# Performance work log

Measured on AMD Instinct MI355X. Metric: run time of the kernel, lower is better.

## Reference

```python
import jax, jax.numpy as jnp
import numpy as np

B = 256          # number of graphs
D = 256          # hidden_dim
H = 4            # num_heads
S = 4            # num_seeds
DH = D // H      # head dim = 64
MAX_NODES = 2048 # max nodes per graph (padding target)


def setup_inputs() -> dict:
    key = jax.random.key(0)
    ks = jax.random.split(key, 8)
    # per-graph node counts, constructed so they sum exactly to B*1024 = 262144
    rng = np.random.RandomState(0)
    delta = rng.randint(0, 960, size=B // 2)
    counts = np.concatenate([1024 + delta, 1024 - delta]).astype(np.int32)
    N = int(counts.sum())  # 262144
    return {
        "node_feat": jax.random.normal(ks[0], (N, D), dtype=jnp.float32),
        "batch_num_nodes": jnp.asarray(counts),
        "seeds": jax.random.normal(ks[1], (S, D), dtype=jnp.float32),
        "in_proj_w": jax.random.normal(ks[2], (3 * D, D), dtype=jnp.float32) * 0.02,
        "in_proj_b": jnp.zeros((3 * D,), jnp.float32),
        "out_proj_w": jax.random.normal(ks[3], (D, D), dtype=jnp.float32) * 0.02,
        "out_proj_b": jnp.zeros((D,), jnp.float32),
        "fc1_w": jax.random.normal(ks[4], (D, S * D), dtype=jnp.float32) * 0.02,
        "fc1_b": jnp.zeros((D,), jnp.float32),
        "fc2_w": jax.random.normal(ks[5], (D, D), dtype=jnp.float32) * 0.02,
        "fc2_b": jnp.zeros((D,), jnp.float32),
    }


def reference(node_feat, batch_num_nodes, seeds, in_proj_w, in_proj_b,
              out_proj_w, out_proj_b, fc1_w, fc1_b, fc2_w, fc2_b):
    N = node_feat.shape[0]
    counts = batch_num_nodes
    # ragged -> padded [B, MAX_NODES, D] via scatter (equiv. of split + zero-pad + stack)
    offsets = jnp.concatenate([jnp.zeros((1,), counts.dtype), jnp.cumsum(counts)[:-1]])
    gid = jnp.repeat(jnp.arange(B, dtype=counts.dtype), counts, total_repeat_length=N)
    pos = jnp.arange(N, dtype=counts.dtype) - offsets[gid]
    padded = jnp.zeros((B, MAX_NODES, D), node_feat.dtype).at[gid, pos].set(node_feat)
    pad_mask = jnp.arange(MAX_NODES)[None, :] >= counts[:, None]  # True = padding key

    # torch nn.MultiheadAttention: packed in_proj split into q/k/v
    Wq, Wk, Wv = jnp.split(in_proj_w, 3, axis=0)
    bq, bk, bv = jnp.split(in_proj_b, 3)
    q = (seeds @ Wq.T + bq).reshape(S, H, DH)                 # [S,H,DH] (broadcast over B)
    k = (padded @ Wk.T + bk).reshape(B, MAX_NODES, H, DH)     # [B,M,H,DH]
    v = (padded @ Wv.T + bv).reshape(B, MAX_NODES, H, DH)

    scale = 1.0 / jnp.sqrt(jnp.asarray(DH, q.dtype))
    scores = jnp.einsum('shd,bmhd->bhsm', q, k) * scale       # [B,H,S,M]
    scores = jnp.where(pad_mask[:, None, None, :], jnp.asarray(-1e9, scores.dtype), scores)
    attn = jax.nn.softmax(scores, axis=-1)
    ctx = jnp.einsum('bhsm,bmhd->bshd', attn, v).reshape(B, S, D)
    attended = ctx @ out_proj_w.T + out_proj_b                # [B,S,D]

    # output_proj: Linear(S*D, D) -> GELU(exact) -> Linear(D, D)
    flat = attended.reshape(B, S * D)
    h = jax.nn.gelu(flat @ fc1_w.T + fc1_b, approximate=False)
    return h @ fc2_w.T + fc2_b                                # [B,D]
```

## Files before the change

### kernel.cpp

```cpp
#include <hip/hip_runtime.h>

#define D 256
#define SH 16
#define Ss 4
#define CH 256
#define NT 64
#define XS_STRIDE 272
#define WB_STRIDE 80

typedef _Float16 half8 __attribute__((ext_vector_type(8)));
typedef _Float16 half4 __attribute__((ext_vector_type(4)));
typedef float f32x4 __attribute__((ext_vector_type(4)));

#define OFF_AF16   ((size_t)0)
#define OFF_CM     ((size_t)8192)
#define OFF_Q      ((size_t)8448)
#define OFF_DESC   ((size_t)12544)
#define OFF_SUMEXP ((size_t)33280)
#define OFF_ACC    ((size_t)49664)
#define OFF_WVT    ((size_t)4243968)
#define OFF_WOT    ((size_t)4506112)
#define OFF_FC1T   ((size_t)4768256)
#define OFF_FC2T   ((size_t)5816832)

__global__ void k_prep(const float* __restrict__ seeds,
                       const float* __restrict__ inw,
                       const float* __restrict__ inb,
                       const int* __restrict__ counts,
                       char* __restrict__ ws) {
  int t = threadIdx.x;
  if (blockIdx.x < 4) {
    int s = blockIdx.x;
    __shared__ float sv[D];
    sv[t] = seeds[s * D + t];
    __syncthreads();
    const float4* wr = (const float4*)(inw + (size_t)t * D);
    float acc = inb[t];
    #pragma unroll 8
    for (int j = 0; j < 64; j++) {
      float4 w4 = wr[j];
      acc += w4.x * sv[4*j] + w4.y * sv[4*j+1] + w4.z * sv[4*j+2] + w4.w * sv[4*j+3];
    }
    ((float*)(ws + OFF_Q))[s * D + t] = acc;
  } else {
    __shared__ int s1[256], s2[256];
    int cnt = counts[t];
    int nch = (cnt + CH - 1) / CH;
    s1[t] = cnt; s2[t] = nch;
    __syncthreads();
    for (int off = 1; off < 256; off <<= 1) {
      int a1 = (t >= off) ? s1[t - off] : 0;
      int a2 = (t >= off) ? s2[t - off] : 0;
      __syncthreads();
      s1[t] += a1; s2[t] += a2;
      __syncthreads();
    }
    int start = s1[t] - cnt, cb = s2[t] - nch;
    int4* desc = (int4*)(ws + OFF_DESC + 16);
    for (int j = 0; j < nch; j++) {
      int nn = cnt - j * CH; if (nn > CH) nn = CH;
      desc[cb + j] = make_int4(t, start + j * CH, nn, 0);
    }
    if (t == 255) *(int*)(ws + OFF_DESC) = s2[255];
  }
}

__global__ void k_mk_a(const float* __restrict__ inw, char* __restrict__ ws) {
  int sh = blockIdx.x;
  int s = sh >> 2, h = sh & 3;
  int j = threadIdx.x;
  __shared__ float qh[64];
  __shared__ float red[256];
  if (j < 64) qh[j] = ((const float*)(ws + OFF_Q))[s * D + h * 64 + j];
  __syncthreads();
  const float* wk = inw + (size_t)(D + h * 64) * D;
  float a = 0.f;
  #pragma unroll 8
  for (int d = 0; d < 64; d++) a += qh[d] * wk[(size_t)d * D + j];
  a *= 0.125f;
  ((_Float16*)(ws + OFF_AF16))[sh * D + j] = (_Float16)a;
  red[j] = a * a;
  __syncthreads();
  for (int st = 128; st > 0; st >>= 1) { if (j < st) red[j] += red[j + st]; __syncthreads(); }
  if (j == 0) ((float*)(ws + OFF_CM))[sh] = -6.0f * sqrtf(red[0]);
}

__global__ void k_transpose(const float* __restrict__ inw, const float* __restrict__ ow,
                            const float* __restrict__ f1w, const float* __restrict__ f2w,
                            char* __restrict__ ws) {
  int b = blockIdx.x;
  const float* src; float* dst; int R, C, ti, tj;
  if (b < 64)       { src = inw + (size_t)512 * D; dst = (float*)(ws + OFF_WVT);  R = 256; C = 256;  int x = b;        tj = x / 8;  ti = x % 8; }
  else if (b < 128) { src = ow;                    dst = (float*)(ws + OFF_WOT);  R = 256; C = 256;  int x = b - 64;   tj = x / 8;  ti = x % 8; }
  else if (b < 192) { src = f2w;                   dst = (float*)(ws + OFF_FC2T); R = 256; C = 256;  int x = b - 128;  tj = x / 8;  ti = x % 8; }
  else              { src = f1w;                   dst = (float*)(ws + OFF_FC1T); R = 256; C = 1024; int x = b - 192;  tj = x / 8;  ti = x % 8; }
  __shared__ float tl[32][33];
  int tx = threadIdx.x & 31, ty = threadIdx.x >> 5;
  #pragma unroll
  for (int k = 0; k < 4; k++) {
    int r = ty + k * 8;
    tl[r][tx] = src[(size_t)(ti * 32 + r) * C + tj * 32 + tx];
  }
  __syncthreads();
  #pragma unroll
  for (int k = 0; k < 4; k++) {
    int r = ty + k * 8;
    dst[(size_t)(tj * 32 + r) * R + ti * 32 + tx] = tl[tx][r];
  }
}

__launch_bounds__(256, 4)
__global__ void k_main(const float* __restrict__ nf, char* __restrict__ ws) {
  int nchunks = *(const int*)(ws + OFF_DESC);
  if ((int)blockIdx.x >= nchunks) return;
  int4 dsc = ((const int4*)(ws + OFF_DESC + 16))[blockIdx.x];
  int g = dsc.x, start = dsc.y, cnt = dsc.z;

  __shared__ _Float16 xs[NT * XS_STRIDE];
  __shared__ _Float16 wb[SH * WB_STRIDE];

  int t = threadIdx.x;
  int lane = t & 63, wv = t >> 6;
  int col = lane & 15, q = lane >> 4;

  const _Float16* af = (const _Float16*)(ws + OFF_AF16);
  half8 aw[8];
  #pragma unroll
  for (int kc = 0; kc < 8; kc++) aw[kc] = *(const half8*)(af + col * D + kc * 32 + q * 8);
  float cmv = ((const float*)(ws + OFF_CM))[col];

  f32x4 acc[4] = {{0,0,0,0},{0,0,0,0},{0,0,0,0},{0,0,0,0}};
  float dsum = 0.f;

  int ntile = (cnt + NT - 1) / NT;
  for (int tile = 0; tile < ntile; tile++) {
    #pragma unroll 4
    for (int p = 0; p < 16; p++) {
      int flat = p * 256 + t;
      int row = flat >> 6, c4 = flat & 63;
      int nloc = tile * NT + row;
      float4 v = make_float4(0.f, 0.f, 0.f, 0.f);
      if (nloc < cnt) v = ((const float4*)(nf + (size_t)(start + nloc) * D))[c4];
      half4 hv;
      hv[0] = (_Float16)v.x; hv[1] = (_Float16)v.y; hv[2] = (_Float16)v.z; hv[3] = (_Float16)v.w;
      *(half4*)(xs + row * XS_STRIDE + c4 * 4) = hv;
    }
    __syncthreads();

    f32x4 sc = {0, 0, 0, 0};
    const _Float16* xrow = xs + (wv * 16 + col) * XS_STRIDE + q * 8;
    #pragma unroll
    for (int kc = 0; kc < 8; kc++) {
      half8 xa = *(const half8*)(xrow + kc * 32);
      sc = __builtin_amdgcn_mfma_f32_16x16x32_f16(xa, aw[kc], sc, 0, 0, 0);
    }
    #pragma unroll
    for (int r = 0; r < 4; r++) {
      int nloc = wv * 16 + q * 4 + r;
      float arg = fminf(sc[r] + cmv, 10.f);
      float wj = (tile * NT + nloc < cnt) ? __expf(arg) : 0.f;
      _Float16 wh = (_Float16)wj;
      dsum += (float)wh;
      wb[col * WB_STRIDE + nloc] = wh;
    }
    __syncthreads();

    #pragma unroll
    for (int ks = 0; ks < 2; ks++) {
      half8 wa = *(const half8*)(wb + col * WB_STRIDE + ks * 32 + q * 8);
      #pragma unroll
      for (int dt = 0; dt < 4; dt++) {
        int dd = wv * 64 + dt * 16 + col;
        half8 xb;
        #pragma unroll
        for (int jj = 0; jj < 8; jj++) xb[jj] = xs[(ks * 32 + q * 8 + jj) * XS_STRIDE + dd];
        acc[dt] = __builtin_amdgcn_mfma_f32_16x16x32_f16(wa, xb, acc[dt], 0, 0, 0);
      }
    }
    __syncthreads();
  }

  dsum += __shfl_xor(dsum, 16);
  dsum += __shfl_xor(dsum, 32);
  if (q == 0) atomicAdd(((float*)(ws + OFF_SUMEXP)) + g * SH + col, dsum);
  float* accw = (float*)(ws + OFF_ACC);
  #pragma unroll
  for (int dt = 0; dt < 4; dt++)
    #pragma unroll
    for (int r = 0; r < 4; r++)
      atomicAdd(&accw[(size_t)(g * SH + q * 4 + r) * D + wv * 64 + dt * 16 + col], acc[dt][r]);
}

__global__ void k_final(const float* __restrict__ inb, const float* __restrict__ ob,
                        const float* __restrict__ f1b, const float* __restrict__ f2b,
                        const char* __restrict__ ws, float* __restrict__ out) {
  int t = threadIdx.x;
  int g0 = blockIdx.x * 2;
  const float* sume = (const float*)(ws + OFF_SUMEXP);
  const float* accw = (const float*)(ws + OFF_ACC);
  const float* WvT = (const float*)(ws + OFF_WVT);
  const float* WoT = (const float*)(ws + OFF_WOT);
  const float* F1T = (const float*)(ws + OFF_FC1T);
  const float* F2T = (const float*)(ws + OFF_FC2T);

  __shared__ float xb2[2][SH][D];
  __shared__ float cx2[2][Ss][D];
  __shared__ float fl2[2][1024];
  __shared__ float hh2[2][D];
  __shared__ float inv[32];

  if (t < 32) inv[t] = 1.0f / sume[(g0 + (t >> 4)) * SH + (t & 15)];
  __syncthreads();
  for (int e = t; e < 2 * SH * D; e += 256) {
    int gg = e >> 12, sh = (e >> 8) & 15, d = e & 255;
    xb2[gg][sh][d] = accw[(size_t)(g0 + gg) * SH * D + sh * D + d] * inv[gg * 16 + sh];
  }
  __syncthreads();

  {
    float ca[2][4] = {{0,0,0,0},{0,0,0,0}};
    int h = t >> 6;
    for (int d = 0; d < D; d++) {
      float wvd = WvT[(size_t)d * D + t];
      #pragma unroll
      for (int gg = 0; gg < 2; gg++)
        #pragma unroll
        for (int s = 0; s < 4; s++)
          ca[gg][s] += wvd * xb2[gg][s * 4 + h][d];
    }
    float bv = inb[2 * D + t];
    #pragma unroll
    for (int gg = 0; gg < 2; gg++)
      #pragma unroll
      for (int s = 0; s < 4; s++) cx2[gg][s][t] = ca[gg][s] + bv;
  }
  __syncthreads();
  {
    float aa[2][4] = {{0,0,0,0},{0,0,0,0}};
    for (int d = 0; d < D; d++) {
      float wod = WoT[(size_t)d * D + t];
      #pragma unroll
      for (int gg = 0; gg < 2; gg++)
        #pragma unroll
        for (int s = 0; s < 4; s++)
          aa[gg][s] += wod * cx2[gg][s][d];
    }
    float bo = ob[t];
    #pragma unroll
    for (int gg = 0; gg < 2; gg++)
      #pragma unroll
      for (int s = 0; s < 4; s++) fl2[gg][s * D + t] = aa[gg][s] + bo;
  }
  __syncthreads();
  {
    float f1[2] = {0, 0};
    for (int k = 0; k < 1024; k++) {
      float w1 = F1T[(size_t)k * D + t];
      f1[0] += w1 * fl2[0][k];
      f1[1] += w1 * fl2[1][k];
    }
    #pragma unroll
    for (int gg = 0; gg < 2; gg++) {
      float x = f1[gg] + f1b[t];
      hh2[gg][t] = 0.5f * x * (1.0f + erff(x * 0.70710678118654752f));
    }
  }
  __syncthreads();
  {
    float f2[2] = {0, 0};
    for (int d = 0; d < D; d++) {
      float w2 = F2T[(size_t)d * D + t];
      f2[0] += w2 * hh2[0][d];
      f2[1] += w2 * hh2[1][d];
    }
    #pragma unroll
    for (int gg = 0; gg < 2; gg++) out[(size_t)(g0 + gg) * D + t] = f2[gg] + f2b[t];
  }
}

extern "C" void kernel_launch(void* const* d_in, const int* in_sizes, int n_in,
                              void* d_out, int out_size, void* d_ws, size_t ws_size,
                              hipStream_t stream) {
  const float* nf    = (const float*)d_in[0];
  const int*   cnts  = (const int*)d_in[1];
  const float* seeds = (const float*)d_in[2];
  const float* inw   = (const float*)d_in[3];
  const float* inb   = (const float*)d_in[4];
  const float* ow    = (const float*)d_in[5];
  const float* obv   = (const float*)d_in[6];
  const float* f1w   = (const float*)d_in[7];
  const float* f1b   = (const float*)d_in[8];
  const float* f2w   = (const float*)d_in[9];
  const float* f2b   = (const float*)d_in[10];
  char* ws = (char*)d_ws;
  float* out = (float*)d_out;
  int N = in_sizes[0] / D;

  hipMemsetAsync(ws + OFF_SUMEXP, 0, (size_t)16384 + 4194304, stream);
  k_prep<<<5, 256, 0, stream>>>(seeds, inw, inb, cnts, ws);
  k_mk_a<<<16, 256, 0, stream>>>(inw, ws);
  k_transpose<<<448, 256, 0, stream>>>(inw, ow, f1w, f2w, ws);
  int maxc = (N + CH - 1) / CH + 256;
  k_main<<<maxc, 256, 0, stream>>>(nf, ws);
  k_final<<<128, 256, 0, stream>>>(inb, obv, f1b, f2b, ws, out);
}
```

Measured before the change: 550.1 us.

## Fuse all stages into one persistent cooperative kernel with grid syncs

Replaces the memset and five separate launches with a single cooperative kernel. It zeroes the workspace, runs prep, query-key precompute and weight transposes, then processes chunks in a grid-stride loop and does the final MLP one graph per block, with grid.sync between phases. The aim is to remove launch gaps and the tail imbalance of the chunk kernel. In exchange the grid is fixed at the occupancy-bounded block count (assumes 256 CUs), and the final stage uses only 256 blocks with one graph each, so the transposed weights are read twice as often.

```diff
diff --git a/kernel.cpp b/kernel.cpp
--- a/kernel.cpp
+++ b/kernel.cpp
@@ -1,4 +1,7 @@
 #include <hip/hip_runtime.h>
+#include <hip/hip_cooperative_groups.h>
+
+namespace cg = cooperative_groups;
 
 #define D 256
 #define SH 16
@@ -14,7 +17,6 @@
 
 #define OFF_AF16   ((size_t)0)
 #define OFF_CM     ((size_t)8192)
-#define OFF_Q      ((size_t)8448)
 #define OFF_DESC   ((size_t)12544)
 #define OFF_SUMEXP ((size_t)33280)
 #define OFF_ACC    ((size_t)49664)
@@ -23,27 +25,88 @@
 #define OFF_FC1T   ((size_t)4768256)
 #define OFF_FC2T   ((size_t)5816832)
 
-__global__ void k_prep(const float* __restrict__ seeds,
-                       const float* __restrict__ inw,
-                       const float* __restrict__ inb,
-                       const int* __restrict__ counts,
-                       char* __restrict__ ws) {
-  int t = threadIdx.x;
-  if (blockIdx.x < 4) {
-    int s = blockIdx.x;
-    __shared__ float sv[D];
-    sv[t] = seeds[s * D + t];
-    __syncthreads();
-    const float4* wr = (const float4*)(inw + (size_t)t * D);
-    float acc = inb[t];
+#define SMEM_BYTES (NT * XS_STRIDE * 2 + SH * WB_STRIDE * 2)
+
+__launch_bounds__(256, 4)
+__global__ void k_all(const float* __restrict__ nf,
+                      const int* __restrict__ counts,
+                      const float* __restrict__ seeds,
+                      const float* __restrict__ inw,
+                      const float* __restrict__ inb,
+                      const float* __restrict__ ow,
+                      const float* __restrict__ obv,
+                      const float* __restrict__ f1w,
+                      const float* __restrict__ f1b,
+                      const float* __restrict__ f2w,
+                      const float* __restrict__ f2b,
+                      char* __restrict__ ws,
+                      float* __restrict__ out) {
+  __shared__ __align__(16) char smem[SMEM_BYTES];
+  cg::grid_group grid = cg::this_grid();
+  const int t = threadIdx.x;
+  const int b = blockIdx.x;
+  const int nblk = gridDim.x;
+
+  {
+    f32x4* z = (f32x4*)(ws + OFF_SUMEXP);
+    const int total4 = (16384 + 4194304) / 16;
+    f32x4 zero = {0.f, 0.f, 0.f, 0.f};
+    for (int i = b * 256 + t; i < total4; i += nblk * 256) z[i] = zero;
+  }
+
+  if (b < 448) {
+    const float* src; float* dst; int R, C, ti, tj;
+    if (b < 64)       { src = inw + (size_t)512 * D; dst = (float*)(ws + OFF_WVT);  R = 256; C = 256;  int x = b;       tj = x / 8; ti = x % 8; }
+    else if (b < 128) { src = ow;                    dst = (float*)(ws + OFF_WOT);  R = 256; C = 256;  int x = b - 64;  tj = x / 8; ti = x % 8; }
+    else if (b < 192) { src = f2w;                   dst = (float*)(ws + OFF_FC2T); R = 256; C = 256;  int x = b - 128; tj = x / 8; ti = x % 8; }
+    else              { src = f1w;                   dst = (float*)(ws + OFF_FC1T); R = 256; C = 1024; int x = b - 192; tj = x / 8; ti = x % 8; }
+    float (*tl)[33] = (float(*)[33])smem;
+    int tx = t & 31, ty = t >> 5;
+    #pragma unroll
+    for (int k = 0; k < 4; k++) {
+      int r = ty + k * 8;
+      tl[r][tx] = src[(size_t)(ti * 32 + r) * C + tj * 32 + tx];
+    }
+    __syncthreads();
+    #pragma unroll
+    for (int k = 0; k < 4; k++) {
+      int r = ty + k * 8;
+      dst[(size_t)(tj * 32 + r) * R + ti * 32 + tx] = tl[tx][r];
+    }
+  } else if (b < 464) {
+    int sh = b - 448, s = sh >> 2, h = sh & 3;
+    float* sd   = (float*)smem;
+    float* part = sd + 256;
+    float* qh   = part + 256;
+    float* red  = qh + 64;
+    sd[t] = seeds[s * D + t];
+    __syncthreads();
+    int j = t & 63, p = t >> 6;
+    const float4* wq = (const float4*)(inw + (size_t)(h * 64 + j) * D + p * 64);
+    float pa = 0.f;
+    #pragma unroll
+    for (int k4 = 0; k4 < 16; k4++) {
+      float4 w4 = wq[k4];
+      pa += w4.x * sd[p*64 + 4*k4] + w4.y * sd[p*64 + 4*k4 + 1]
+          + w4.z * sd[p*64 + 4*k4 + 2] + w4.w * sd[p*64 + 4*k4 + 3];
+    }
+    part[p * 64 + j] = pa;
+    __syncthreads();
+    if (t < 64) qh[t] = part[t] + part[64 + t] + part[128 + t] + part[192 + t] + inb[h * 64 + t];
+    __syncthreads();
+    const float* wk = inw + (size_t)(D + h * 64) * D;
+    float a = 0.f;
     #pragma unroll 8
-    for (int j = 0; j < 64; j++) {
-      float4 w4 = wr[j];
-      acc += w4.x * sv[4*j] + w4.y * sv[4*j+1] + w4.z * sv[4*j+2] + w4.w * sv[4*j+3];
-    }
-    ((float*)(ws + OFF_Q))[s * D + t] = acc;
-  } else {
-    __shared__ int s1[256], s2[256];
+    for (int d = 0; d < 64; d++) a += qh[d] * wk[(size_t)d * D + t];
+    a *= 0.125f;
+    ((_Float16*)(ws + OFF_AF16))[sh * D + t] = (_Float16)a;
+    red[t] = a * a;
+    __syncthreads();
+    for (int st = 128; st > 0; st >>= 1) { if (t < st) red[t] += red[t + st]; __syncthreads(); }
+    if (t == 0) ((float*)(ws + OFF_CM))[sh] = -6.0f * sqrtf(red[0]);
+  } else if (b == 464) {
+    int* s1 = (int*)smem;
+    int* s2 = s1 + 256;
     int cnt = counts[t];
     int nch = (cnt + CH - 1) / CH;
     s1[t] = cnt; s2[t] = nch;
@@ -57,224 +120,173 @@
     }
     int start = s1[t] - cnt, cb = s2[t] - nch;
     int4* desc = (int4*)(ws + OFF_DESC + 16);
-    for (int j = 0; j < nch; j++) {
-      int nn = cnt - j * CH; if (nn > CH) nn = CH;
-      desc[cb + j] = make_int4(t, start + j * CH, nn, 0);
+    for (int jj = 0; jj < nch; jj++) {
+      int nn = cnt - jj * CH; if (nn > CH) nn = CH;
+      desc[cb + jj] = make_int4(t, start + jj * CH, nn, 0);
     }
     if (t == 255) *(int*)(ws + OFF_DESC) = s2[255];
   }
-}
-
-__global__ void k_mk_a(const float* __restrict__ inw, char* __restrict__ ws) {
-  int sh = blockIdx.x;
-  int s = sh >> 2, h = sh & 3;
-  int j = threadIdx.x;
-  __shared__ float qh[64];
-  __shared__ float red[256];
-  if (j < 64) qh[j] = ((const float*)(ws + OFF_Q))[s * D + h * 64 + j];
-  __syncthreads();
-  const float* wk = inw + (size_t)(D + h * 64) * D;
-  float a = 0.f;
-  #pragma unroll 8
-  for (int d = 0; d < 64; d++) a += qh[d] * wk[(size_t)d * D + j];
-  a *= 0.125f;
-  ((_Float16*)(ws + OFF_AF16))[sh * D + j] = (_Float16)a;
-  red[j] = a * a;
-  __syncthreads();
-  for (int st = 128; st > 0; st >>= 1) { if (j < st) red[j] += red[j + st]; __syncthreads(); }
-  if (j == 0) ((float*)(ws + OFF_CM))[sh] = -6.0f * sqrtf(red[0]);
-}
-
-__global__ void k_transpose(const float* __restrict__ inw, const float* __restrict__ ow,
-                            const float* __restrict__ f1w, const float* __restrict__ f2w,
-                            char* __restrict__ ws) {
-  int b = blockIdx.x;
-  const float* src; float* dst; int R, C, ti, tj;
-  if (b < 64)       { src = inw + (size_t)512 * D; dst = (float*)(ws + OFF_WVT);  R = 256; C = 256;  int x = b;        tj = x / 8;  ti = x % 8; }
-  else if (b < 128) { src = ow;                    dst = (float*)(ws + OFF_WOT);  R = 256; C = 256;  int x = b - 64;   tj = x / 8;  ti = x % 8; }
-  else if (b < 192) { src = f2w;                   dst = (float*)(ws + OFF_FC2T); R = 256; C = 256;  int x = b - 128;  tj = x / 8;  ti = x % 8; }
-  else              { src = f1w;                   dst = (float*)(ws + OFF_FC1T); R = 256; C = 1024; int x = b - 192;  tj = x / 8;  ti = x % 8; }
-  __shared__ float tl[32][33];
-  int tx = threadIdx.x & 31, ty = threadIdx.x >> 5;
-  #pragma unroll
-  for (int k = 0; k < 4; k++) {
-    int r = ty + k * 8;
-    tl[r][tx] = src[(size_t)(ti * 32 + r) * C + tj * 32 + tx];
-  }
-  __syncthreads();
-  #pragma unroll
-  for (int k = 0; k < 4; k++) {
-    int r = ty + k * 8;
-    dst[(size_t)(tj * 32 + r) * R + ti * 32 + tx] = tl[tx][r];
-  }
-}
-
-__launch_bounds__(256, 4)
-__global__ void k_main(const float* __restrict__ nf, char* __restrict__ ws) {
-  int nchunks = *(const int*)(ws + OFF_DESC);
-  if ((int)blockIdx.x >= nchunks) return;
-  int4 dsc = ((const int4*)(ws + OFF_DESC + 16))[blockIdx.x];
-  int g = dsc.x, start = dsc.y, cnt = dsc.z;
-
-  __shared__ _Float16 xs[NT * XS_STRIDE];
-  __shared__ _Float16 wb[SH * WB_STRIDE];
-
-  int t = threadIdx.x;
-  int lane = t & 63, wv = t >> 6;
-  int col = lane & 15, q = lane >> 4;
-
-  const _Float16* af = (const _Float16*)(ws + OFF_AF16);
-  half8 aw[8];
-  #pragma unroll
-  for (int kc = 0; kc < 8; kc++) aw[kc] = *(const half8*)(af + col * D + kc * 32 + q * 8);
-  float cmv = ((const float*)(ws + OFF_CM))[col];
-
-  f32x4 acc[4] = {{0,0,0,0},{0,0,0,0},{0,0,0,0},{0,0,0,0}};
-  float dsum = 0.f;
-
-  int ntile = (cnt + NT - 1) / NT;
-  for (int tile = 0; tile < ntile; tile++) {
-    #pragma unroll 4
-    for (int p = 0; p < 16; p++) {
-      int flat = p * 256 + t;
-      int row = flat >> 6, c4 = flat & 63;
-      int nloc = tile * NT + row;
-      float4 v = make_float4(0.f, 0.f, 0.f, 0.f);
-      if (nloc < cnt) v = ((const float4*)(nf + (size_t)(start + nloc) * D))[c4];
-      half4 hv;
-      hv[0] = (_Float16)v.x; hv[1] = (_Float16)v.y; hv[2] = (_Float16)v.z; hv[3] = (_Float16)v.w;
-      *(half4*)(xs + row * XS_STRIDE + c4 * 4) = hv;
-    }
-    __syncthreads();
-
-    f32x4 sc = {0, 0, 0, 0};
-    const _Float16* xrow = xs + (wv * 16 + col) * XS_STRIDE + q * 8;
-    #pragma unroll
-    for (int kc = 0; kc < 8; kc++) {
-      half8 xa = *(const half8*)(xrow + kc * 32);
-      sc = __builtin_amdgcn_mfma_f32_16x16x32_f16(xa, aw[kc], sc, 0, 0, 0);
-    }
-    #pragma unroll
-    for (int r = 0; r < 4; r++) {
-      int nloc = wv * 16 + q * 4 + r;
-      float arg = fminf(sc[r] + cmv, 10.f);
-      float wj = (tile * NT + nloc < cnt) ? __expf(arg) : 0.f;
-      _Float16 wh = (_Float16)wj;
-      dsum += (float)wh;
-      wb[col * WB_STRIDE + nloc] = wh;
-    }
-    __syncthreads();
-
-    #pragma unroll
-    for (int ks = 0; ks < 2; ks++) {
-      half8 wa = *(const half8*)(wb + col * WB_STRIDE + ks * 32 + q * 8);
+
+  __threadfence();
+  grid.sync();
+  __threadfence();
+
+  {
+    _Float16* xs = (_Float16*)smem;
+    _Float16* wb = (_Float16*)(smem + NT * XS_STRIDE * 2);
+    const int lane = t & 63, wv = t >> 6;
+    const int col = lane & 15, q = lane >> 4;
+
+    const _Float16* af = (const _Float16*)(ws + OFF_AF16);
+    half8 aw[8];
+    #pragma unroll
+    for (int kc = 0; kc < 8; kc++) aw[kc] = *(const half8*)(af + col * D + kc * 32 + q * 8);
+    const float cmv = ((const float*)(ws + OFF_CM))[col];
+    const int nchunks = *(const int*)(ws + OFF_DESC);
+    float* sume = (float*)(ws + OFF_SUMEXP);
+    float* accw = (float*)(ws + OFF_ACC);
+    const int4* descp = (const int4*)(ws + OFF_DESC + 16);
+
+    for (int c = b; c < nchunks; c += nblk) {
+      int4 dsc = descp[c];
+      int g = dsc.x, start = dsc.y, cnt = dsc.z;
+
+      f32x4 acc[4] = {{0,0,0,0},{0,0,0,0},{0,0,0,0},{0,0,0,0}};
+      float dsum = 0.f;
+
+      int ntile = (cnt + NT - 1) / NT;
+      for (int tile = 0; tile < ntile; tile++) {
+        #pragma unroll 4
+        for (int p = 0; p < 16; p++) {
+          int flat = p * 256 + t;
+          int row = flat >> 6, c4 = flat & 63;
+          int nloc = tile * NT + row;
+          float4 v = make_float4(0.f, 0.f, 0.f, 0.f);
+          if (nloc < cnt) v = ((const float4*)(nf + (size_t)(start + nloc) * D))[c4];
+          half4 hv;
+          hv[0] = (_Float16)v.x; hv[1] = (_Float16)v.y; hv[2] = (_Float16)v.z; hv[3] = (_Float16)v.w;
+          *(half4*)(xs + row * XS_STRIDE + c4 * 4) = hv;
+        }
+        __syncthreads();
+
+        f32x4 sc = {0, 0, 0, 0};
+        const _Float16* xrow = xs + (wv * 16 + col) * XS_STRIDE + q * 8;
+        #pragma unroll
+        for (int kc = 0; kc < 8; kc++) {
+          half8 xa = *(const half8*)(xrow + kc * 32);
+          sc = __builtin_amdgcn_mfma_f32_16x16x32_f16(xa, aw[kc], sc, 0, 0, 0);
+        }
+        #pragma unroll
+        for (int r = 0; r < 4; r++) {
+          int nloc = wv * 16 + q * 4 + r;
+          float arg = fminf(sc[r] + cmv, 10.f);
+          float wj = (tile * NT + nloc < cnt) ? __expf(arg) : 0.f;
+          _Float16 wh = (_Float16)wj;
+          dsum += (float)wh;
+          wb[col * WB_STRIDE + nloc] = wh;
+        }
+        __syncthreads();
+
+        #pragma unroll
+        for (int ks = 0; ks < 2; ks++) {
+          half8 wa = *(const half8*)(wb + col * WB_STRIDE + ks * 32 + q * 8);
+          #pragma unroll
+          for (int dt = 0; dt < 4; dt++) {
+            int dd = wv * 64 + dt * 16 + col;
+            half8 xb;
+            #pragma unroll
+            for (int jj = 0; jj < 8; jj++) xb[jj] = xs[(ks * 32 + q * 8 + jj) * XS_STRIDE + dd];
+            acc[dt] = __builtin_amdgcn_mfma_f32_16x16x32_f16(wa, xb, acc[dt], 0, 0, 0);
+          }
+        }
+        __syncthreads();
+      }
+
+      float ds = dsum;
+      ds += __shfl_xor(ds, 16);
+      ds += __shfl_xor(ds, 32);
+      if (q == 0) atomicAdd(sume + g * SH + col, ds);
       #pragma unroll
-      for (int dt = 0; dt < 4; dt++) {
-        int dd = wv * 64 + dt * 16 + col;
-        half8 xb;
-        #pragma unroll
-        for (int jj = 0; jj < 8; jj++) xb[jj] = xs[(ks * 32 + q * 8 + jj) * XS_STRIDE + dd];
-        acc[dt] = __builtin_amdgcn_mfma_f32_16x16x32_f16(wa, xb, acc[dt], 0, 0, 0);
-      }
-    }
-    __syncthreads();
-  }
-
-  dsum += __shfl_xor(dsum, 16);
-  dsum += __shfl_xor(dsum, 32);
-  if (q == 0) atomicAdd(((float*)(ws + OFF_SUMEXP)) + g * SH + col, dsum);
-  float* accw = (float*)(ws + OFF_ACC);
-  #pragma unroll
-  for (int dt = 0; dt < 4; dt++)
-    #pragma unroll
-    for (int r = 0; r < 4; r++)
-      atomicAdd(&accw[(size_t)(g * SH + q * 4 + r) * D + wv * 64 + dt * 16 + col], acc[dt][r]);
-}
-
-__global__ void k_final(const float* __restrict__ inb, const float* __restrict__ ob,
-                        const float* __restrict__ f1b, const float* __restrict__ f2b,
-                        const char* __restrict__ ws, float* __restrict__ out) {
-  int t = threadIdx.x;
-  int g0 = blockIdx.x * 2;
-  const float* sume = (const float*)(ws + OFF_SUMEXP);
-  const float* accw = (const float*)(ws + OFF_ACC);
-  const float* WvT = (const float*)(ws + OFF_WVT);
-  const float* WoT = (const float*)(ws + OFF_WOT);
-  const float* F1T = (const float*)(ws + OFF_FC1T);
-  const float* F2T = (const float*)(ws + OFF_FC2T);
-
-  __shared__ float xb2[2][SH][D];
-  __shared__ float cx2[2][Ss][D];
-  __shared__ float fl2[2][1024];
-  __shared__ float hh2[2][D];
-  __shared__ float inv[32];
-
-  if (t < 32) inv[t] = 1.0f / sume[(g0 + (t >> 4)) * SH + (t & 15)];
-  __syncthreads();
-  for (int e = t; e < 2 * SH * D; e += 256) {
-    int gg = e >> 12, sh = (e >> 8) & 15, d = e & 255;
-    xb2[gg][sh][d] = accw[(size_t)(g0 + gg) * SH * D + sh * D + d] * inv[gg * 16 + sh];
-  }
-  __syncthreads();
-
-  {
-    float ca[2][4] = {{0,0,0,0},{0,0,0,0}};
-    int h = t >> 6;
-    for (int d = 0; d < D; d++) {
-      float wvd = WvT[(size_t)d * D + t];
+      for (int dt = 0; dt < 4; dt++)
+        #pragma unroll
+        for (int r = 0; r < 4; r++)
+          atomicAdd(&accw[(size_t)(g * SH + q * 4 + r) * D + wv * 64 + dt * 16 + col], acc[dt][r]);
+    }
+  }
+
+  __threadfence();
+  grid.sync();
+  __threadfence();
+
+  if (b < 256) {
+    const int g = b;
+    const float* sume = (const float*)(ws + OFF_SUMEXP);
+    const float* accw = (const float*)(ws + OFF_ACC);
+    const float* WvT = (const float*)(ws + OFF_WVT);
+    const float* WoT = (const float*)(ws + OFF_WOT);
+    const float* F1T = (const float*)(ws + OFF_FC1T);
+    const float* F2T = (const float*)(ws + OFF_FC2T);
+    float* xb  = (float*)smem;
+    float* cx  = xb + 16 * 256;
+    float* fl  = cx + 4 * 256;
+    float* hh  = fl + 1024;
+    float* inv = hh + 256;
+
+    if (t < 16) inv[t] = 1.0f / sume[g * SH + t];
+    __syncthreads();
+    #pragma unroll
+    for (int sh = 0; sh < 16; sh++)
+      xb[sh * 256 + t] = accw[(size_t)g * (SH * D) + sh * D + t] * inv[sh];
+    __syncthreads();
+
+    const int h = t >> 6;
+    {
+      float ca[4] = {0, 0, 0, 0};
+      #pragma unroll 4
+      for (int d = 0; d < 256; d++) {
+        float wvd = WvT[(size_t)d * D + t];
+        #pragma unroll
+        for (int s = 0; s < 4; s++) ca[s] += wvd * xb[(s * 4 + h) * 256 + d];
+      }
+      float bv = inb[2 * D + t];
       #pragma unroll
-      for (int gg = 0; gg < 2; gg++)
-        #pragma unroll
-        for (int s = 0; s < 4; s++)
-          ca[gg][s] += wvd * xb2[gg][s * 4 + h][d];
-    }
-    float bv = inb[2 * D + t];
-    #pragma unroll
-    for (int gg = 0; gg < 2; gg++)
+      for (int s = 0; s < 4; s++) cx[s * 256 + t] = ca[s] + bv;
+    }
+    __syncthreads();
+    {
+      float aa[4] = {0, 0, 0, 0};
+      #pragma unroll 4
+      for (int d = 0; d < 256; d++) {
+        float wod = WoT[(size_t)d * D + t];
+        #pragma unroll
+        for (int s = 0; s < 4; s++) aa[s] += wod * cx[s * 256 + d];
+      }
+      float bo = obv[t];
       #pragma unroll
-      for (int s = 0; s < 4; s++) cx2[gg][s][t] = ca[gg][s] + bv;
-  }
-  __syncthreads();
-  {
-    float aa[2][4] = {{0,0,0,0},{0,0,0,0}};
-    for (int d = 0; d < D; d++) {
-      float wod = WoT[(size_t)d * D + t];
-      #pragma unroll
-      for (int gg = 0; gg < 2; gg++)
-        #pragma unroll
-        for (int s = 0; s < 4; s++)
-          aa[gg][s] += wod * cx2[gg][s][d];
-    }
-    float bo = ob[t];
-    #pragma unroll
-    for (int gg = 0; gg < 2; gg++)
-      #pragma unroll
-      for (int s = 0; s < 4; s++) fl2[gg][s * D + t] = aa[gg][s] + bo;
-  }
-  __syncthreads();
-  {
-    float f1[2] = {0, 0};
-    for (int k = 0; k < 1024; k++) {
-      float w1 = F1T[(size_t)k * D + t];
-      f1[0] += w1 * fl2[0][k];
-      f1[1] += w1 * fl2[1][k];
-    }
-    #pragma unroll
-    for (int gg = 0; gg < 2; gg++) {
-      float x = f1[gg] + f1b[t];
-      hh2[gg][t] = 0.5f * x * (1.0f + erff(x * 0.70710678118654752f));
-    }
-  }
-  __syncthreads();
-  {
-    float f2[2] = {0, 0};
-    for (int d = 0; d < D; d++) {
-      float w2 = F2T[(size_t)d * D + t];
-      f2[0] += w2 * hh2[0][d];
-      f2[1] += w2 * hh2[1][d];
-    }
-    #pragma unroll
-    for (int gg = 0; gg < 2; gg++) out[(size_t)(g0 + gg) * D + t] = f2[gg] + f2b[t];
+      for (int s = 0; s < 4; s++) fl[s * 256 + t] = aa[s] + bo;
+    }
+    __syncthreads();
+    {
+      float f1p[4] = {0, 0, 0, 0};
+      #pragma unroll 2
+      for (int k = 0; k < 256; k++) {
+        #pragma unroll
+        for (int p = 0; p < 4; p++)
+          f1p[p] += F1T[(size_t)(p * 256 + k) * D + t] * fl[p * 256 + k];
+      }
+      float x = f1p[0] + f1p[1] + f1p[2] + f1p[3] + f1b[t];
+      hh[t] = 0.5f * x * (1.0f + erff(x * 0.70710678118654752f));
+    }
+    __syncthreads();
+    {
+      float f2a = 0.f, f2c = 0.f;
+      #pragma unroll 4
+      for (int d = 0; d < 256; d += 2) {
+        f2a += F2T[(size_t)d * D + t] * hh[d];
+        f2c += F2T[(size_t)(d + 1) * D + t] * hh[d + 1];
+      }
+      out[(size_t)g * D + t] = f2a + f2c + f2b[t];
+    }
   }
 }
 
@@ -294,13 +306,18 @@
   const float* f2b   = (const float*)d_in[10];
   char* ws = (char*)d_ws;
   float* out = (float*)d_out;
-  int N = in_sizes[0] / D;
-
-  hipMemsetAsync(ws + OFF_SUMEXP, 0, (size_t)16384 + 4194304, stream);
-  k_prep<<<5, 256, 0, stream>>>(seeds, inw, inb, cnts, ws);
-  k_mk_a<<<16, 256, 0, stream>>>(inw, ws);
-  k_transpose<<<448, 256, 0, stream>>>(inw, ow, f1w, f2w, ws);
-  int maxc = (N + CH - 1) / CH + 256;
-  k_main<<<maxc, 256, 0, stream>>>(nf, ws);
-  k_final<<<128, 256, 0, stream>>>(inb, obv, f1b, f2b, ws, out);
+
+  static int blocks = 0;
+  if (blocks == 0) {
+    int occ = 0;
+    hipOccupancyMaxActiveBlocksPerMultiprocessor(&occ, (const void*)k_all, 256, 0);
+    if (occ < 2) occ = 2;
+    if (occ > 4) occ = 4;
+    blocks = occ * 256;
+  }
+
+  void* args[] = {(void*)&nf, (void*)&cnts, (void*)&seeds, (void*)&inw, (void*)&inb,
+                  (void*)&ow, (void*)&obv, (void*)&f1w, (void*)&f1b, (void*)&f2w,
+                  (void*)&f2b, (void*)&ws, (void*)&out};
+  hipLaunchCooperativeKernel((void*)k_all, dim3(blocks), dim3(256), args, 0, stream);
 }
```

After: 864.3 us. 1.57x slower.
